# Performance work log

Hardware: AMD Instinct MI355X
Metric: run time of the kernel (lower is better)

## Reference

```python
import jax, jax.numpy as jnp
import numpy as np

B, N, H = 8, 1024, 1024
HEADS, DH = 16, 64  # H = HEADS * DH
LN_EPS = 1e-12


def setup_inputs() -> dict:
    key = jax.random.key(0)
    ks = jax.random.split(key, 8)
    s = 0.02
    return {
        "hidden_states": jax.random.normal(ks[0], (B, N, H), jnp.float32),
        "role_mask": jax.random.randint(ks[1], (B, N, N), 0, 2, jnp.int32),
        "conv_len": jax.random.randint(ks[2], (B,), 0, 160, jnp.int32),
        "Wq": jax.random.normal(ks[3], (H, H), jnp.float32) * s,
        "bq": jnp.zeros((H,), jnp.float32),
        "Wk": jax.random.normal(ks[4], (H, H), jnp.float32) * s,
        "bk": jnp.zeros((H,), jnp.float32),
        "Wv": jax.random.normal(ks[5], (H, H), jnp.float32) * s,
        "bv": jnp.zeros((H,), jnp.float32),
        "Wo": jax.random.normal(ks[6], (H, H), jnp.float32) * s,
        "bo": jnp.zeros((H,), jnp.float32),
        "gamma": jnp.ones((H,), jnp.float32),
        "beta": jnp.zeros((H,), jnp.float32),
    }


def _split_heads(x):
    b, n, h = x.shape
    return x.reshape(b, n, HEADS, DH).transpose(0, 2, 1, 3)  # [B,h,N,dh]


def reference(hidden_states, role_mask, conv_len, Wq, bq, Wk, bk, Wv, bv, Wo, bo, gamma, beta):
    q = _split_heads(hidden_states @ Wq + bq)
    k = _split_heads(hidden_states @ Wk + bk)
    v = _split_heads(hidden_states @ Wv + bv)

    scale = 1.0 / jnp.sqrt(jnp.asarray(DH, hidden_states.dtype))
    scores = jnp.einsum("bhqd,bhkd->bhqk", q, k) * scale  # [B,h,N,N]
    scores = jnp.where(role_mask[:, None, :, :] == 0, jnp.asarray(-1e9, scores.dtype), scores)
    probs = jax.nn.softmax(scores, axis=-1)  # dropout is identity in eval

    ctx = jnp.einsum("bhqk,bhkd->bhqd", probs, v)
    ctx = ctx.transpose(0, 2, 1, 3).reshape(hidden_states.shape)  # [B,N,H]

    # output projection + residual + LayerNorm (BERT-style, eps=1e-12)
    y = ctx @ Wo + bo + hidden_states
    mu = jnp.mean(y, axis=-1, keepdims=True)
    var = jnp.mean(jnp.square(y - mu), axis=-1, keepdims=True)
    context_layer = (y - mu) / jnp.sqrt(var + LN_EPS) * gamma + beta

    # state_type == 'user': rows 6*idx+2 (perspective) and 6*idx+3 (emotion)
    bidx = jnp.arange(context_layer.shape[0])
    base = 6 * conv_len
    perspective_taking = context_layer[bidx, base + 2]  # [B,H]
    high_emo_states = context_layer[bidx, base + 3]     # [B,H]
    return context_layer, high_emo_states, perspective_taking
```

## Files before the change

### kernel.cpp

```cpp
#include <hip/hip_runtime.h>
#include <math.h>

#define HN 1024
#define BB 8
#define NN 1024
#define NHEADS 16
#define DH 64
#define M_ROWS (BB * NN)

typedef __attribute__((ext_vector_type(8))) short short8;
typedef __attribute__((ext_vector_type(8))) unsigned short ushort8v;
typedef __attribute__((ext_vector_type(4))) float floatx4;
typedef __attribute__((ext_vector_type(4))) unsigned int uint4v;

__device__ __forceinline__ unsigned short f2bf(float f) {
    unsigned int u = __builtin_bit_cast(unsigned int, f);
    u += 0x7fffu + ((u >> 16) & 1u);
    return (unsigned short)(u >> 16);
}

__device__ __forceinline__ unsigned int pack2bf(float a, float b) {
    return (unsigned int)f2bf(a) | ((unsigned int)f2bf(b) << 16);
}

__device__ __forceinline__ void gload16(const unsigned short* g, unsigned short* l) {
    __builtin_amdgcn_global_load_lds(
        (const __attribute__((address_space(1))) void*)g,
        (__attribute__((address_space(3))) void*)l, 16, 0, 0);
}

__global__ __launch_bounds__(256)
void cvt_hs_k(const float* __restrict__ in, unsigned short* __restrict__ out)
{
    int i = (blockIdx.x * 256 + threadIdx.x) * 4;
    float4 v = *(const float4*)(in + i);
    ushort4 o;
    o.x = f2bf(v.x); o.y = f2bf(v.y); o.z = f2bf(v.z); o.w = f2bf(v.w);
    *(ushort4*)&out[i] = o;
}

__global__ __launch_bounds__(256)
void cvt_wT4_k(const float* __restrict__ W0, const float* __restrict__ W1,
               const float* __restrict__ W2, const float* __restrict__ W3,
               unsigned short* __restrict__ o0, unsigned short* __restrict__ o1,
               unsigned short* __restrict__ o2, unsigned short* __restrict__ o3)
{
    __shared__ float Ls[32][33];
    const int z = blockIdx.z;
    const float* W = z == 0 ? W0 : (z == 1 ? W1 : (z == 2 ? W2 : W3));
    unsigned short* out = z == 0 ? o0 : (z == 1 ? o1 : (z == 2 ? o2 : o3));
    const int t = threadIdx.x;
    const int k0 = blockIdx.x * 32, n0 = blockIdx.y * 32;
    const int r = t >> 3, c4 = (t & 7) * 4;
    float4 v = *(const float4*)(W + (size_t)(k0 + r) * HN + n0 + c4);
    Ls[r][c4 + 0] = v.x; Ls[r][c4 + 1] = v.y;
    Ls[r][c4 + 2] = v.z; Ls[r][c4 + 3] = v.w;
    __syncthreads();
    ushort4 o;
    o.x = f2bf(Ls[c4 + 0][r]); o.y = f2bf(Ls[c4 + 1][r]);
    o.z = f2bf(Ls[c4 + 2][r]); o.w = f2bf(Ls[c4 + 3][r]);
    *(ushort4*)&out[(size_t)(n0 + r) * HN + k0 + c4] = o;
}

__global__ __launch_bounds__(256)
void mfma_gemm_k(const unsigned short* __restrict__ A,
                 const unsigned short* __restrict__ Bt,
                 const float* __restrict__ b0p, const float* __restrict__ b1p,
                 const float* __restrict__ b2p,
                 const float* __restrict__ resid,
                 unsigned short* __restrict__ Qb, unsigned short* __restrict__ Kb,
                 unsigned short* __restrict__ Vtb, float* __restrict__ Yb,
                 int mode)
{
    __shared__ unsigned short smem[128 * 136];
    unsigned short* As = smem;
    unsigned short* Bs = smem + 4096;

    const int tid  = threadIdx.x;
    const int wave = tid >> 6, lane = tid & 63;
    const int quad = lane >> 4, n16 = lane & 15;
    const int wm = wave >> 1, wn = wave & 1;
    const int row0 = blockIdx.x * 128;
    const int n0   = blockIdx.y * 128;

    floatx4 acc[4][4];
    #pragma unroll
    for (int mi = 0; mi < 4; ++mi)
        #pragma unroll
        for (int ni = 0; ni < 4; ++ni)
            acc[mi][ni] = (floatx4){0.f, 0.f, 0.f, 0.f};

    const unsigned short* ga = A  + (size_t)(row0 + wave * 32 + (lane >> 2)) * 1024 + (lane & 3) * 8;
    const unsigned short* gb = Bt + (size_t)(n0  + wave * 32 + (lane >> 2)) * 1024 + (lane & 3) * 8;

    for (int k0 = 0; k0 < 1024; k0 += 32) {
        gload16(ga,             As + wave * 1024);
        gload16(ga + 16 * 1024, As + wave * 1024 + 512);
        gload16(gb,             Bs + wave * 1024);
        gload16(gb + 16 * 1024, Bs + wave * 1024 + 512);
        ga += 32; gb += 32;
        __syncthreads();

        short8 a[4], b[4];
        #pragma unroll
        for (int mi = 0; mi < 4; ++mi)
            a[mi] = *(const short8*)&As[(wm * 64 + mi * 16 + n16) * 32 + quad * 8];
        #pragma unroll
        for (int ni = 0; ni < 4; ++ni)
            b[ni] = *(const short8*)&Bs[(wn * 64 + ni * 16 + n16) * 32 + quad * 8];
        #pragma unroll
        for (int mi = 0; mi < 4; ++mi)
            #pragma unroll
            for (int ni = 0; ni < 4; ++ni)
                acc[mi][ni] = __builtin_amdgcn_mfma_f32_16x16x32_bf16(
                    a[mi], b[ni], acc[mi][ni], 0, 0, 0);
        __syncthreads();
    }

    if (mode == 0) {
        const int sel = n0 >> 10;
        const int c0  = n0 & 1023;
        const float* bias = sel == 0 ? b0p : (sel == 1 ? b1p : b2p);
        float bvv[4];
        #pragma unroll
        for (int ni = 0; ni < 4; ++ni)
            bvv[ni] = bias[c0 + wn * 64 + ni * 16 + n16];

        #pragma unroll
        for (int mi = 0; mi < 4; ++mi)
            #pragma unroll
            for (int ni = 0; ni < 4; ++ni)
                #pragma unroll
                for (int r = 0; r < 4; ++r)
                    smem[(wm * 64 + mi * 16 + quad * 4 + r) * 136 +
                         wn * 64 + ni * 16 + n16] = f2bf(acc[mi][ni][r] + bvv[ni]);
        __syncthreads();

        if (sel < 2) {
            unsigned short* outb = sel == 0 ? Qb : Kb;
            #pragma unroll
            for (int i = 0; i < 8; ++i) {
                int c = i * 256 + tid;
                int r = c >> 4;
                int colc = (c & 15) * 8;
                ushort8v v = *(const ushort8v*)&smem[r * 136 + colc];
                int row = row0 + r, bb = row >> 10, nn = row & 1023;
                int gc = c0 + colc, head = gc >> 6, d = gc & 63;
                *(ushort8v*)&outb[(((size_t)bb * NHEADS + head) * NN + nn) * DH + d] = v;
            }
        } else {
            #pragma unroll
            for (int i = 0; i < 8; ++i) {
                int c = i * 256 + tid;
                int dcol = c >> 4;
                int nnc = (c & 15) * 8;
                ushort8v v;
                #pragma unroll
                for (int j = 0; j < 8; ++j)
                    v[j] = smem[(nnc + j) * 136 + dcol];
                int gc = c0 + dcol, head = gc >> 6, d = gc & 63;
                int row = row0 + nnc, bb = row >> 10, nn = row & 1023;
                *(ushort8v*)&Vtb[(((size_t)bb * NHEADS + head) * DH + d) * NN + nn] = v;
            }
        }
    } else {
        float bvv[4];
        #pragma unroll
        for (int ni = 0; ni < 4; ++ni)
            bvv[ni] = b0p[n0 + wn * 64 + ni * 16 + n16];
        #pragma unroll
        for (int mi = 0; mi < 4; ++mi)
            #pragma unroll
            for (int r = 0; r < 4; ++r) {
                int row = row0 + wm * 64 + mi * 16 + quad * 4 + r;
                const float* rr = resid + (size_t)row * HN;
                float* yr = Yb + (size_t)row * HN;
                #pragma unroll
                for (int ni = 0; ni < 4; ++ni) {
                    int col = n0 + wn * 64 + ni * 16 + n16;
                    yr[col] = acc[mi][ni][r] + bvv[ni] + rr[col];
                }
            }
    }
}

__global__ __launch_bounds__(256)
void attn_mfma_k(const unsigned short* __restrict__ Q,
                 const unsigned short* __restrict__ K,
                 const unsigned short* __restrict__ Vt,
                 const int* __restrict__ mask,
                 unsigned short* __restrict__ ctx)
{
    __shared__ unsigned short KsB[2 * 4096];
    __shared__ unsigned short VsB[2 * 4096];

    const int tid  = threadIdx.x;
    const int wave = tid >> 6, lane = tid & 63;
    const int quad = lane >> 4, n16 = lane & 15;
    const int sw   = n16 & 7;
    const int b  = blockIdx.x;
    const int q0 = blockIdx.y << 7;
    const int h  = blockIdx.z;
    const int bh = b * NHEADS + h;
    const int qw = q0 + wave * 32;

    short8 aq[2][2];
    #pragma unroll
    for (int qh = 0; qh < 2; ++qh) {
        const unsigned short* qp = Q + ((size_t)bh * NN + qw + qh * 16 + n16) * DH;
        aq[qh][0] = *(const short8*)(qp + quad * 8);
        aq[qh][1] = *(const short8*)(qp + 32 + quad * 8);
    }

    floatx4 O[2][4];
    #pragma unroll
    for (int qh = 0; qh < 2; ++qh)
        #pragma unroll
        for (int d4 = 0; d4 < 4; ++d4)
            O[qh][d4] = (floatx4){0.f, 0.f, 0.f, 0.f};
    float lsum[2] = {0.f, 0.f};

    const unsigned short* Kg = K  + (size_t)bh * NN * DH;
    const unsigned short* Vg = Vt + (size_t)bh * DH * NN;

    const int r8 = lane >> 3;
    const int cs = (lane & 7) ^ (r8 & 7);
    const int gk0 = ((wave >> 1) << 5) + ((r8 >> 2) << 3) + ((wave & 1) << 2) + (r8 & 3);
    const unsigned short* kg0 = Kg + (size_t)gk0 * DH + cs * 8;
    const unsigned short* kg1 = kg0 + 16 * DH;
    const unsigned short* vg0 = Vg + (size_t)(wave * 16 + r8) * NN + cs * 8;
    const unsigned short* vg1 = vg0 + 8 * NN;
    unsigned short* lk = KsB + wave * 1024;
    unsigned short* lv = VsB + wave * 1024;

    const int* mp0 = mask + ((size_t)b * NN + qw + n16) * NN + quad * 8;
    const int* mp1 = mp0 + 16 * NN;

    gload16(kg0, lk);  gload16(kg1, lk + 512);
    gload16(vg0, lv);  gload16(vg1, lv + 512);

    for (int t = 0; t < 16; ++t) {
        __syncthreads();
        const int cur = t & 1;
        if (t < 15) {
            const int nxt = cur ^ 1;
            kg0 += 4096; kg1 += 4096; vg0 += 64; vg1 += 64;
            gload16(kg0, lk + nxt * 4096); gload16(kg1, lk + nxt * 4096 + 512);
            gload16(vg0, lv + nxt * 4096); gload16(vg1, lv + nxt * 4096 + 512);
        }
        const unsigned short* Kc = KsB + cur * 4096;
        const unsigned short* Vc = VsB + cur * 4096;
        const int kbase = t * 64;

        int4 m4a[2][4];
        #pragma unroll
        for (int kt = 0; kt < 4; ++kt) {
            const int moff = kbase + ((kt >> 1) << 5) + ((kt & 1) << 2);
            m4a[0][kt] = *(const int4*)(mp0 + moff);
            m4a[1][kt] = *(const int4*)(mp1 + moff);
        }

        unsigned int pk[2][8];
        #pragma unroll
        for (int kt = 0; kt < 4; ++kt) {
            const unsigned short* kr = Kc + (kt * 16 + n16) * 64;
            short8 kf0 = *(const short8*)&kr[(quad ^ sw) * 8];
            short8 kf1 = *(const short8*)&kr[((quad + 4) ^ sw) * 8];
            #pragma unroll
            for (int qh = 0; qh < 2; ++qh) {
                floatx4 s = (floatx4){0.f, 0.f, 0.f, 0.f};
                s = __builtin_amdgcn_mfma_f32_16x16x32_bf16(kf0, aq[qh][0], s, 0, 0, 0);
                s = __builtin_amdgcn_mfma_f32_16x16x32_bf16(kf1, aq[qh][1], s, 0, 0, 0);
                int4 m4 = m4a[qh][kt];
                float p0 = m4.x ? __expf(s[0] * 0.125f) : 0.f;
                float p1 = m4.y ? __expf(s[1] * 0.125f) : 0.f;
                float p2 = m4.z ? __expf(s[2] * 0.125f) : 0.f;
                float p3 = m4.w ? __expf(s[3] * 0.125f) : 0.f;
                lsum[qh] += (p0 + p1) + (p2 + p3);
                pk[qh][kt * 2]     = pack2bf(p0, p1);
                pk[qh][kt * 2 + 1] = pack2bf(p2, p3);
            }
        }

        #pragma unroll
        for (int c = 0; c < 2; ++c) {
            short8 vb[4];
            #pragma unroll
            for (int d4 = 0; d4 < 4; ++d4)
                vb[d4] = *(const short8*)&Vc[(d4 * 16 + n16) * 64 +
                                             ((4 * c + quad) ^ sw) * 8];
            #pragma unroll
            for (int qh = 0; qh < 2; ++qh) {
                uint4v u = {pk[qh][c * 4], pk[qh][c * 4 + 1],
                            pk[qh][c * 4 + 2], pk[qh][c * 4 + 3]};
                short8 pb = __builtin_bit_cast(short8, u);
                #pragma unroll
                for (int d4 = 0; d4 < 4; ++d4)
                    O[qh][d4] = __builtin_amdgcn_mfma_f32_16x16x32_bf16(
                        vb[d4], pb, O[qh][d4], 0, 0, 0);
            }
        }
    }

    #pragma unroll
    for (int qh = 0; qh < 2; ++qh) {
        float ltot = lsum[qh];
        ltot += __shfl_xor(ltot, 16);
        ltot += __shfl_xor(ltot, 32);
        const float inv = 1.0f / ltot;
        unsigned short* cp = ctx + ((size_t)b * NN + qw + qh * 16 + n16) * HN
                             + h * DH + quad * 4;
        #pragma unroll
        for (int d4 = 0; d4 < 4; ++d4) {
            unsigned int u01 = pack2bf(O[qh][d4][0] * inv, O[qh][d4][1] * inv);
            unsigned int u23 = pack2bf(O[qh][d4][2] * inv, O[qh][d4][3] * inv);
            *(uint2*)(cp + d4 * 16) = (uint2){u01, u23};
        }
    }
}

__global__ __launch_bounds__(256)
void ln_ext_k(const float* __restrict__ y, const float* __restrict__ gamma,
              const float* __restrict__ beta, const int* __restrict__ conv_len,
              float* __restrict__ out, float* __restrict__ he, float* __restrict__ pt)
{
    const int row = blockIdx.x;
    const int t = threadIdx.x;
    float4 v = ((const float4*)(y + (size_t)row * HN))[t];
    float s  = v.x + v.y + v.z + v.w;
    float s2 = v.x * v.x + v.y * v.y + v.z * v.z + v.w * v.w;
    #pragma unroll
    for (int off = 32; off > 0; off >>= 1) {
        s  += __shfl_down(s, off);
        s2 += __shfl_down(s2, off);
    }
    __shared__ float ws1[4], ws2[4];
    __shared__ float smu, sinv;
    if ((t & 63) == 0) { ws1[t >> 6] = s; ws2[t >> 6] = s2; }
    __syncthreads();
    if (t == 0) {
        float ts  = ws1[0] + ws1[1] + ws1[2] + ws1[3];
        float ts2 = ws2[0] + ws2[1] + ws2[2] + ws2[3];
        float mu  = ts * (1.0f / 1024.0f);
        float var = ts2 * (1.0f / 1024.0f) - mu * mu;
        smu  = mu;
        sinv = 1.0f / sqrtf(var + 1e-12f);
    }
    __syncthreads();
    const float mu = smu, inv = sinv;
    float4 g = ((const float4*)gamma)[t];
    float4 be = ((const float4*)beta)[t];
    float4 o;
    o.x = (v.x - mu) * inv * g.x + be.x;
    o.y = (v.y - mu) * inv * g.y + be.y;
    o.z = (v.z - mu) * inv * g.z + be.z;
    o.w = (v.w - mu) * inv * g.w + be.w;
    ((float4*)(out + (size_t)row * HN))[t] = o;

    const int b = row >> 10, n = row & 1023;
    const int base = 6 * conv_len[b];
    if (n == base + 3) ((float4*)(he + (size_t)b * HN))[t] = o;
    if (n == base + 2) ((float4*)(pt + (size_t)b * HN))[t] = o;
}

extern "C" void kernel_launch(void* const* d_in, const int* in_sizes, int n_in,
                              void* d_out, int out_size, void* d_ws, size_t ws_size,
                              hipStream_t stream)
{
    const float* hs    = (const float*)d_in[0];
    const int*   mask  = (const int*)d_in[1];
    const int*   clen  = (const int*)d_in[2];
    const float* Wq    = (const float*)d_in[3];
    const float* bq    = (const float*)d_in[4];
    const float* Wk    = (const float*)d_in[5];
    const float* bk    = (const float*)d_in[6];
    const float* Wv    = (const float*)d_in[7];
    const float* bv    = (const float*)d_in[8];
    const float* Wo    = (const float*)d_in[9];
    const float* bo    = (const float*)d_in[10];
    const float* gamma = (const float*)d_in[11];
    const float* beta  = (const float*)d_in[12];
    float* out = (float*)d_out;

    unsigned short* Ab  = (unsigned short*)d_ws;
    unsigned short* Wt3 = Ab  + (size_t)M_ROWS * HN;
    unsigned short* Wot = Wt3 + (size_t)3 * HN * HN;
    unsigned short* Qb  = Wot + (size_t)HN * HN;
    unsigned short* Kb  = Qb  + (size_t)M_ROWS * HN;
    unsigned short* Vtb = Kb  + (size_t)M_ROWS * HN;
    unsigned short* Ctx = Vtb + (size_t)M_ROWS * HN;
    float*          Yb  = (float*)Qb;

    dim3 gb(256);

    hipLaunchKernelGGL(cvt_hs_k, dim3((size_t)M_ROWS * HN / 1024), gb, 0, stream, hs, Ab);
    hipLaunchKernelGGL(cvt_wT4_k, dim3(32, 32, 4), gb, 0, stream,
                       Wq, Wk, Wv, Wo,
                       Wt3, Wt3 + (size_t)HN * HN, Wt3 + (size_t)2 * HN * HN, Wot);

    hipLaunchKernelGGL(mfma_gemm_k, dim3(64, 24), gb, 0, stream,
                       Ab, Wt3, bq, bk, bv, (const float*)nullptr,
                       Qb, Kb, Vtb, (float*)nullptr, 0);

    hipLaunchKernelGGL(attn_mfma_k, dim3(BB, NN / 128, NHEADS), gb, 0, stream,
                       Qb, Kb, Vtb, mask, Ctx);

    hipLaunchKernelGGL(mfma_gemm_k, dim3(64, 8), gb, 0, stream,
                       Ctx, Wot, bo, (const float*)nullptr, (const float*)nullptr, hs,
                       (unsigned short*)nullptr, (unsigned short*)nullptr,
                       (unsigned short*)nullptr, Yb, 1);

    float* he = out + (size_t)BB * NN * HN;
    float* pt = he + BB * HN;
    hipLaunchKernelGGL(ln_ext_k, dim3(M_ROWS), gb, 0, stream, Yb, gamma, beta, clen,
                       out, he, pt);
}
```

Measured before the change: 359.8 us.

## Load K and V fragments directly from global memory, dropping LDS double buffering

The attention kernel no longer stages K and V tiles through double-buffered shared memory with __syncthreads. Each wave now reads its MFMA operand fragments for K and V^T straight from global memory, relying on L2 and L1 caching for the reuse across the four waves of a block. This removes the LDS traffic and block-wide barriers, but it duplicates global loads across waves and exposes load latency without an explicit prefetch.

```diff
diff --git a/kernel.cpp b/kernel.cpp
--- a/kernel.cpp
+++ b/kernel.cpp
@@ -191,13 +191,9 @@
                  const int* __restrict__ mask,
                  unsigned short* __restrict__ ctx)
 {
-    __shared__ unsigned short KsB[2 * 4096];
-    __shared__ unsigned short VsB[2 * 4096];
-
     const int tid  = threadIdx.x;
     const int wave = tid >> 6, lane = tid & 63;
     const int quad = lane >> 4, n16 = lane & 15;
-    const int sw   = n16 & 7;
     const int b  = blockIdx.x;
     const int q0 = blockIdx.y << 7;
     const int h  = blockIdx.z;
@@ -220,58 +216,39 @@
             O[qh][d4] = (floatx4){0.f, 0.f, 0.f, 0.f};
     float lsum[2] = {0.f, 0.f};
 
-    const unsigned short* Kg = K  + (size_t)bh * NN * DH;
-    const unsigned short* Vg = Vt + (size_t)bh * DH * NN;
-
-    const int r8 = lane >> 3;
-    const int cs = (lane & 7) ^ (r8 & 7);
-    const int gk0 = ((wave >> 1) << 5) + ((r8 >> 2) << 3) + ((wave & 1) << 2) + (r8 & 3);
-    const unsigned short* kg0 = Kg + (size_t)gk0 * DH + cs * 8;
-    const unsigned short* kg1 = kg0 + 16 * DH;
-    const unsigned short* vg0 = Vg + (size_t)(wave * 16 + r8) * NN + cs * 8;
-    const unsigned short* vg1 = vg0 + 8 * NN;
-    unsigned short* lk = KsB + wave * 1024;
-    unsigned short* lv = VsB + wave * 1024;
-
+    const int krow = ((n16 >> 2) << 3) + (n16 & 3);
+    const unsigned short* Kp = K + (size_t)bh * NN * DH + krow * DH + quad * 8;
+    const unsigned short* Vp = Vt + (size_t)bh * DH * NN + (size_t)n16 * NN + quad * 8;
     const int* mp0 = mask + ((size_t)b * NN + qw + n16) * NN + quad * 8;
     const int* mp1 = mp0 + 16 * NN;
 
-    gload16(kg0, lk);  gload16(kg1, lk + 512);
-    gload16(vg0, lv);  gload16(vg1, lv + 512);
-
     for (int t = 0; t < 16; ++t) {
-        __syncthreads();
-        const int cur = t & 1;
-        if (t < 15) {
-            const int nxt = cur ^ 1;
-            kg0 += 4096; kg1 += 4096; vg0 += 64; vg1 += 64;
-            gload16(kg0, lk + nxt * 4096); gload16(kg1, lk + nxt * 4096 + 512);
-            gload16(vg0, lv + nxt * 4096); gload16(vg1, lv + nxt * 4096 + 512);
-        }
-        const unsigned short* Kc = KsB + cur * 4096;
-        const unsigned short* Vc = VsB + cur * 4096;
-        const int kbase = t * 64;
-
-        int4 m4a[2][4];
+        const int kb = t * 64;
+        const unsigned short* Kt = Kp + (size_t)kb * DH;
+        const unsigned short* Vtp = Vp + kb;
+
+        short8 kf[4][2];
+        kf[0][0] = *(const short8*)(Kt + 0);
+        kf[0][1] = *(const short8*)(Kt + 32);
+        kf[1][0] = *(const short8*)(Kt + 256);
+        kf[1][1] = *(const short8*)(Kt + 288);
+        kf[2][0] = *(const short8*)(Kt + 2048);
+        kf[2][1] = *(const short8*)(Kt + 2080);
+        kf[3][0] = *(const short8*)(Kt + 2304);
+        kf[3][1] = *(const short8*)(Kt + 2336);
+
+        unsigned int pk[2][8];
         #pragma unroll
         for (int kt = 0; kt < 4; ++kt) {
-            const int moff = kbase + ((kt >> 1) << 5) + ((kt & 1) << 2);
-            m4a[0][kt] = *(const int4*)(mp0 + moff);
-            m4a[1][kt] = *(const int4*)(mp1 + moff);
-        }
-
-        unsigned int pk[2][8];
-        #pragma unroll
-        for (int kt = 0; kt < 4; ++kt) {
-            const unsigned short* kr = Kc + (kt * 16 + n16) * 64;
-            short8 kf0 = *(const short8*)&kr[(quad ^ sw) * 8];
-            short8 kf1 = *(const short8*)&kr[((quad + 4) ^ sw) * 8];
+            const int moff = kb + ((kt >> 1) << 5) + ((kt & 1) << 2);
+            int4 m40 = *(const int4*)(mp0 + moff);
+            int4 m41 = *(const int4*)(mp1 + moff);
             #pragma unroll
             for (int qh = 0; qh < 2; ++qh) {
                 floatx4 s = (floatx4){0.f, 0.f, 0.f, 0.f};
-                s = __builtin_amdgcn_mfma_f32_16x16x32_bf16(kf0, aq[qh][0], s, 0, 0, 0);
-                s = __builtin_amdgcn_mfma_f32_16x16x32_bf16(kf1, aq[qh][1], s, 0, 0, 0);
-                int4 m4 = m4a[qh][kt];
+                s = __builtin_amdgcn_mfma_f32_16x16x32_bf16(kf[kt][0], aq[qh][0], s, 0, 0, 0);
+                s = __builtin_amdgcn_mfma_f32_16x16x32_bf16(kf[kt][1], aq[qh][1], s, 0, 0, 0);
+                int4 m4 = qh ? m41 : m40;
                 float p0 = m4.x ? __expf(s[0] * 0.125f) : 0.f;
                 float p1 = m4.y ? __expf(s[1] * 0.125f) : 0.f;
                 float p2 = m4.z ? __expf(s[2] * 0.125f) : 0.f;
@@ -287,8 +264,7 @@
             short8 vb[4];
             #pragma unroll
             for (int d4 = 0; d4 < 4; ++d4)
-                vb[d4] = *(const short8*)&Vc[(d4 * 16 + n16) * 64 +
-                                             ((4 * c + quad) ^ sw) * 8];
+                vb[d4] = *(const short8*)(Vtp + (size_t)(d4 * 16) * NN + c * 32);
             #pragma unroll
             for (int qh = 0; qh < 2; ++qh) {
                 uint4v u = {pk[qh][c * 4], pk[qh][c * 4 + 1],
```

New measurement: 465.5 us. +29.4%, slower.
